# Kernel tuning notes

Measured on AMD Instinct MI355X. Metric: run time of the kernel, lower is better.

Reference implementation:

```python
import jax, jax.numpy as jnp
import numpy as np

N_HEAD = 16


def setup_inputs() -> dict:
    key = jax.random.key(0)
    ks = jax.random.split(key, 5)
    B, T, C = 2, 2048, 1024
    s = 1.0 / np.sqrt(C)
    inp = {
        "x": jax.random.normal(ks[0], (B, T, C), dtype=jnp.float32),
        "Wq": jax.random.normal(ks[1], (C, C), dtype=jnp.float32) * s,
        "bq": jnp.zeros((C,), dtype=jnp.float32),
        "Wk": jax.random.normal(ks[2], (C, C), dtype=jnp.float32) * s,
        "bk": jnp.zeros((C,), dtype=jnp.float32),
        "Wv": jax.random.normal(ks[3], (C, C), dtype=jnp.float32) * s,
        "bv": jnp.zeros((C,), dtype=jnp.float32),
        "Wp": jax.random.normal(ks[4], (C, C), dtype=jnp.float32) * s,
        "bp": jnp.zeros((C,), dtype=jnp.float32),
    }
    return inp


def reference(x, Wq, bq, Wk, bk, Wv, bv, Wp, bp):
    B, T, C = x.shape
    H = N_HEAD
    D = C // H
    # linear projections (torch Linear: x @ W.T + b)
    q = (x @ Wq.T + bq).reshape(B, T, H, D)
    k = (x @ Wk.T + bk).reshape(B, T, H, D)
    v = (x @ Wv.T + bv).reshape(B, T, H, D)
    # scaled dot-product attention (NO causal mask in original forward)
    att = jnp.einsum("bthd,bshd->bhts", q, k) * (1.0 / np.sqrt(D))
    att = jax.nn.softmax(att, axis=-1)
    y = jnp.einsum("bhts,bshd->bthd", att, v).reshape(B, T, C)
    # output projection (dropouts are identity at p=0 / eval)
    return y @ Wp.T + bp
```

## Files before the change

kernel.cpp:

```cpp
#include <hip/hip_runtime.h>
#include <hip/hip_bf16.h>

typedef __attribute__((ext_vector_type(4))) float f32x4;
typedef __attribute__((ext_vector_type(16))) float f32x16;
typedef __attribute__((ext_vector_type(8))) short bf16x8;
typedef __attribute__((ext_vector_type(2))) unsigned int u32x2;

#define T_SEQ 2048
#define C_DIM 1024
#define NH 16
#define DHD 64
#define ROWB 136

__device__ __forceinline__ unsigned cvtpk_bf16(float lo, float hi) {
    unsigned r;
    asm("v_cvt_pk_bf16_f32 %0, %1, %2" : "=v"(r) : "v"(lo), "v"(hi));
    return r;
}

__device__ __forceinline__ float exp2_hw(float x) {
    float r;
    asm("v_exp_f32 %0, %1" : "=v"(r) : "v"(x));
    return r;
}

__device__ __forceinline__ void async_copy16(void* lds, const void* g) {
    __builtin_amdgcn_global_load_lds(
        (const __attribute__((address_space(1))) unsigned int*)(uintptr_t)g,
        (__attribute__((address_space(3))) unsigned int*)(unsigned int)(uintptr_t)lds,
        16, 0, 0);
}

__device__ __forceinline__ bf16x8 ld_frag8(const char* p) {
    union { float2 f[2]; bf16x8 v; } u;
    u.f[0] = *(const float2*)(p);
    u.f[1] = *(const float2*)(p + 8);
    return u.v;
}

__global__ __launch_bounds__(256) void cvt_all(const float* __restrict__ x,
                                               const float* __restrict__ Wq, const float* __restrict__ Wk,
                                               const float* __restrict__ Wv, const float* __restrict__ Wp,
                                               __hip_bfloat16* __restrict__ xb,
                                               __hip_bfloat16* __restrict__ wf,
                                               __hip_bfloat16* __restrict__ wpb) {
    int i = blockIdx.x * blockDim.x + threadIdx.x;
    const float* src; __hip_bfloat16* dst; int off;
    if (i < 1048576) { src = x; dst = xb; off = i; }
    else {
        int j = i - 1048576; int wi = j >> 18; off = j & 262143;
        switch (wi) {
            case 0:  src = Wq; dst = wf;           break;
            case 1:  src = Wk; dst = wf + 1048576; break;
            case 2:  src = Wv; dst = wf + 2097152; break;
            default: src = Wp; dst = wpb;          break;
        }
    }
    float4 v = *(const float4*)(src + (size_t)off * 4);
    union { __hip_bfloat16 h[4]; u32x2 u; } p;
    p.h[0] = __float2bfloat16(v.x); p.h[1] = __float2bfloat16(v.y);
    p.h[2] = __float2bfloat16(v.z); p.h[3] = __float2bfloat16(v.w);
    *(u32x2*)(dst + (size_t)off * 4) = p.u;
}

__global__ __launch_bounds__(512) void gemm_qkv(const __hip_bfloat16* __restrict__ A,
                                                const __hip_bfloat16* __restrict__ Bw,
                                                const float* __restrict__ biasq,
                                                const float* __restrict__ biask,
                                                const float* __restrict__ biasv,
                                                __hip_bfloat16* __restrict__ oq,
                                                __hip_bfloat16* __restrict__ okk,
                                                __hip_bfloat16* __restrict__ ovt) {
    __shared__ __align__(16) char lds[131072];

    const int wg = ((int)blockIdx.x & 7) * 32 + ((int)blockIdx.x >> 3);
    const int m0 = (wg & 31) * 128;
    const int n0 = (wg >> 5) * 384;

    const int tid = threadIdx.x;
    const int w = tid >> 6, l = tid & 63;
    const int wr = w >> 2, wc = w & 3;
    const int lg = l >> 4, lr = l & 15;

    const int sr0 = tid >> 3;
    const int sc0 = (tid & 7) * 16;
    const int gc0 = sc0 ^ ((sr0 & 7) << 4);
    const size_t goff = (size_t)sr0 * 2048 + gc0;

    const char* Ag = (const char*)A + (size_t)m0 * 2048;
    const char* Bg = (const char*)Bw + (size_t)n0 * 2048;

    auto STAGE_A = [&](int buf, int half, int kt) {
        const char* g = Ag + (size_t)(half * 64) * 2048 + kt * 128 + goff;
        char* d = lds + (buf * 2 + half) * 8192 + w * 1024;
        async_copy16(d, g);
    };
    auto STAGE_B = [&](int buf, int half, int kt) {
        #pragma unroll
        for (int p = 0; p < 3; p++) {
            const char* g = Bg + (size_t)(half * 192 + p * 64) * 2048 + kt * 128 + goff;
            char* d = lds + 32768 + (buf * 2 + half) * 24576 + p * 8192 + w * 1024;
            async_copy16(d, g);
        }
    };

    const int sw = (lr & 7) << 4;
    auto LDA = [&](bf16x8* af, int buf) {
        const char* base = lds + (buf * 2 + wr) * 8192;
        #pragma unroll
        for (int m = 0; m < 4; m++) {
            const int r = m * 16 + lr;
            #pragma unroll
            for (int kk = 0; kk < 2; kk++)
                af[m * 2 + kk] = *(const bf16x8*)(base + r * 128 + ((kk * 64 + lg * 16) ^ sw));
        }
    };
    auto LDB = [&](bf16x8* bfv, int buf, int nq) {
        const char* base = lds + 32768 + (buf * 2 + (wc >> 1)) * 24576;
        #pragma unroll
        for (int n = 0; n < 2; n++) {
            const int r = (wc & 1) * 96 + (nq * 2 + n) * 16 + lr;
            #pragma unroll
            for (int kk = 0; kk < 2; kk++)
                bfv[n * 2 + kk] = *(const bf16x8*)(base + r * 128 + ((kk * 64 + lg * 16) ^ sw));
        }
    };

    f32x4 acc[4][6] = {};
    auto MF = [&](const bf16x8* af, const bf16x8* bfv, int nq) {
        #pragma unroll
        for (int m = 0; m < 4; m++)
            #pragma unroll
            for (int n = 0; n < 2; n++)
                #pragma unroll
                for (int kk = 0; kk < 2; kk++)
                    acc[m][nq * 2 + n] = __builtin_amdgcn_mfma_f32_16x16x32_bf16(
                        af[m * 2 + kk], bfv[n * 2 + kk], acc[m][nq * 2 + n], 0, 0, 0);
    };

#define PH_OPEN()  __builtin_amdgcn_sched_barrier(0); \
                   __builtin_amdgcn_s_barrier(); \
                   asm volatile("s_waitcnt lgkmcnt(0)" ::: "memory"); \
                   __builtin_amdgcn_sched_barrier(0); \
                   __builtin_amdgcn_s_setprio(1);
#define PH_CLOSE() __builtin_amdgcn_s_setprio(0); \
                   __builtin_amdgcn_sched_barrier(0); \
                   __builtin_amdgcn_s_barrier();
#define PH_CLOSE_VM2() __builtin_amdgcn_s_setprio(0); \
                   asm volatile("s_waitcnt vmcnt(2)" ::: "memory"); \
                   __builtin_amdgcn_sched_barrier(0); \
                   __builtin_amdgcn_s_barrier();
#define PH_CLOSE_VM5() __builtin_amdgcn_s_setprio(0); \
                   asm volatile("s_waitcnt vmcnt(5)" ::: "memory"); \
                   __builtin_amdgcn_sched_barrier(0); \
                   __builtin_amdgcn_s_barrier();

    bf16x8 af[8], bfA[4], bfB[4], bfC[4];

    STAGE_B(0, 0, 0); STAGE_B(0, 1, 0); STAGE_A(0, 0, 0); STAGE_A(0, 1, 0);
    STAGE_A(1, 0, 1); STAGE_A(1, 1, 1); STAGE_B(1, 0, 1);
    asm volatile("s_waitcnt vmcnt(5)" ::: "memory");
    __builtin_amdgcn_sched_barrier(0);
    __builtin_amdgcn_s_barrier();

    for (int it = 0; it < 8; ++it) {
        const int t1 = 2 * it + 1;
        const int c2 = (2 * it + 2 < 16) ? 2 * it + 2 : 14;
        const int c3 = (2 * it + 3 < 16) ? 2 * it + 3 : 15;
        const int b2 = c2 & 1, b3 = c3 & 1;

        LDA(af, 0); LDB(bfA, 0, 0);
        STAGE_B(1, 1, t1);
        PH_OPEN(); MF(af, bfA, 0); PH_CLOSE();
        LDB(bfB, 0, 1);
        STAGE_A(b2, 0, c2); STAGE_A(b2, 1, c2);
        PH_OPEN(); MF(af, bfB, 1); PH_CLOSE();
        LDB(bfC, 0, 2);
        PH_OPEN(); MF(af, bfC, 2); PH_CLOSE_VM2();

        LDA(af, 1); LDB(bfA, 1, 0);
        STAGE_B(b2, 0, c2);
        PH_OPEN(); MF(af, bfA, 0); PH_CLOSE();
        LDB(bfB, 1, 1);
        STAGE_B(b2, 1, c2); STAGE_A(b3, 0, c3); STAGE_A(b3, 1, c3);
        PH_OPEN(); MF(af, bfB, 1); PH_CLOSE();
        LDB(bfC, 1, 2);
        STAGE_B(b3, 0, c3);
        PH_OPEN(); MF(af, bfC, 2); PH_CLOSE_VM5();
    }
#undef PH_OPEN
#undef PH_CLOSE
#undef PH_CLOSE_VM2
#undef PH_CLOSE_VM5

    #pragma unroll
    for (int m = 0; m < 4; m++) {
        const int rowb = m0 + wr * 64 + m * 16 + lg * 4;
        const int b = rowb >> 11, t0r = rowb & 2047;
        #pragma unroll
        for (int nf = 0; nf < 6; nf++) {
            const int col = n0 + wc * 96 + nf * 16 + lr;
            const int proj = col >> 10;
            const int colL = col & 1023;
            const int hh = colL >> 6, dd = colL & 63;
            if (proj < 2) {
                const float* bias = (proj == 0) ? biasq : biask;
                const float bsc = (proj == 0) ? 0.125f * 1.4426950408889634f : 1.0f;
                __hip_bfloat16* dst = (proj == 0) ? oq : okk;
                #pragma unroll
                for (int rr = 0; rr < 4; rr++) {
                    const int row = rowb + rr;
                    float val = (acc[m][nf][rr] + bias[colL]) * bsc;
                    dst[(((size_t)(b * NH + hh)) * T_SEQ + (row & 2047)) * DHD + dd] = __float2bfloat16(val);
                }
            } else {
                const float bv = biasv[colL];
                union { __hip_bfloat16 h[4]; u32x2 u; } p;
                #pragma unroll
                for (int rr = 0; rr < 4; rr++)
                    p.h[rr] = __float2bfloat16(acc[m][nf][rr] + bv);
                *(u32x2*)&ovt[(((size_t)(b * NH + hh)) * DHD + dd) * T_SEQ + t0r] = p.u;
            }
        }
    }
}

__global__ __launch_bounds__(512) void gemm_proj2(const __hip_bfloat16* __restrict__ A,
                                                  const __hip_bfloat16* __restrict__ Bw,
                                                  const float* __restrict__ biasp,
                                                  float* __restrict__ outf) {
    __shared__ __align__(16) char lds[65536];

    const int wg = ((int)blockIdx.x & 7) * 32 + ((int)blockIdx.x >> 3);
    const int m0 = (wg & 31) * 128;
    const int n0 = (wg >> 5) * 128;

    const int tid = threadIdx.x;
    const int w = tid >> 6, l = tid & 63;
    const int wr = w >> 2, wc = w & 3;
    const int lg = l >> 4, lr = l & 15;

    const int sr0 = tid >> 3;
    const int sc0 = (tid & 7) * 16;
    const int gc0 = sc0 ^ ((sr0 & 7) << 4);
    const size_t goff = (size_t)sr0 * 2048 + gc0;

    const char* Ag = (const char*)A + (size_t)m0 * 2048;
    const char* Bg = (const char*)Bw + (size_t)n0 * 2048;

    auto STAGE_A = [&](int buf, int half, int kt) {
        const char* g = Ag + (size_t)(half * 64) * 2048 + kt * 128 + goff;
        char* d = lds + (buf * 2 + half) * 8192 + w * 1024;
        async_copy16(d, g);
    };
    auto STAGE_B = [&](int buf, int half, int kt) {
        const char* g = Bg + (size_t)(half * 64) * 2048 + kt * 128 + goff;
        char* d = lds + 32768 + (buf * 2 + half) * 8192 + w * 1024;
        async_copy16(d, g);
    };

    const int sw = (lr & 7) << 4;
    auto LDA = [&](bf16x8* af, int buf) {
        const char* base = lds + (buf * 2 + wr) * 8192;
        #pragma unroll
        for (int m = 0; m < 4; m++) {
            const int r = m * 16 + lr;
            #pragma unroll
            for (int kk = 0; kk < 2; kk++)
                af[m * 2 + kk] = *(const bf16x8*)(base + r * 128 + ((kk * 64 + lg * 16) ^ sw));
        }
    };
    auto LDB = [&](bf16x8* bfv, int buf, int n) {
        const char* base = lds + 32768 + (buf * 2 + (wc >> 1)) * 8192;
        const int r = (wc & 1) * 32 + n * 16 + lr;
        #pragma unroll
        for (int kk = 0; kk < 2; kk++)
            bfv[kk] = *(const bf16x8*)(base + r * 128 + ((kk * 64 + lg * 16) ^ sw));
    };

    f32x4 acc[4][2] = {};
    auto MF = [&](const bf16x8* af, const bf16x8* bfv, int n) {
        #pragma unroll
        for (int m = 0; m < 4; m++)
            #pragma unroll
            for (int kk = 0; kk < 2; kk++)
                acc[m][n] = __builtin_amdgcn_mfma_f32_16x16x32_bf16(
                    af[m * 2 + kk], bfv[kk], acc[m][n], 0, 0, 0);
    };

#define PH_OPEN()  __builtin_amdgcn_sched_barrier(0); \
                   __builtin_amdgcn_s_barrier(); \
                   asm volatile("s_waitcnt lgkmcnt(0)" ::: "memory"); \
                   __builtin_amdgcn_sched_barrier(0); \
                   __builtin_amdgcn_s_setprio(1);
#define PH_CLOSE() __builtin_amdgcn_s_setprio(0); \
                   __builtin_amdgcn_sched_barrier(0); \
                   __builtin_amdgcn_s_barrier();
#define PH_CLOSE_VM2() __builtin_amdgcn_s_setprio(0); \
                   asm volatile("s_waitcnt vmcnt(2)" ::: "memory"); \
                   __builtin_amdgcn_sched_barrier(0); \
                   __builtin_amdgcn_s_barrier();

    bf16x8 af[8], bf0[2], bf1[2];

    STAGE_B(0, 0, 0); STAGE_B(0, 1, 0); STAGE_A(0, 0, 0); STAGE_A(0, 1, 0);
    STAGE_A(1, 0, 1); STAGE_A(1, 1, 1);
    asm volatile("s_waitcnt vmcnt(2)" ::: "memory");
    __builtin_amdgcn_sched_barrier(0);
    __builtin_amdgcn_s_barrier();

    for (int it = 0; it < 8; ++it) {
        const int t1 = 2 * it + 1;
        const int c2 = (2 * it + 2 < 16) ? 2 * it + 2 : 14;
        const int c3 = (2 * it + 3 < 16) ? 2 * it + 3 : 15;
        const int b2 = c2 & 1, b3 = c3 & 1;

        LDA(af, 0); LDB(bf0, 0, 0);
        STAGE_B(1, 0, t1); STAGE_B(1, 1, t1);
        PH_OPEN(); MF(af, bf0, 0); PH_CLOSE();
        LDB(bf1, 0, 1);
        STAGE_A(b2, 0, c2); STAGE_A(b2, 1, c2);
        PH_OPEN(); MF(af, bf1, 1); PH_CLOSE_VM2();

        LDA(af, 1); LDB(bf0, 1, 0);
        STAGE_B(b2, 0, c2); STAGE_B(b2, 1, c2);
        PH_OPEN(); MF(af, bf0, 0); PH_CLOSE();
        LDB(bf1, 1, 1);
        STAGE_A(b3, 0, c3); STAGE_A(b3, 1, c3);
        PH_OPEN(); MF(af, bf1, 1); PH_CLOSE_VM2();
    }
#undef PH_OPEN
#undef PH_CLOSE
#undef PH_CLOSE_VM2

    #pragma unroll
    for (int m = 0; m < 4; m++)
        #pragma unroll
        for (int n = 0; n < 2; n++)
            #pragma unroll
            for (int r = 0; r < 4; r++) {
                int row = m0 + wr * 64 + m * 16 + lg * 4 + r;
                int col = n0 + wc * 32 + n * 16 + lr;
                outf[(size_t)row * C_DIM + col] = acc[m][n][r] + biasp[col];
            }
}

__global__ __launch_bounds__(256) void attn12(const __hip_bfloat16* __restrict__ Q,
                                              const __hip_bfloat16* __restrict__ K,
                                              const __hip_bfloat16* __restrict__ Vt,
                                              __hip_bfloat16* __restrict__ Y) {
    const int bid = blockIdx.x;
    const int xcd = bid & 7, slot = bid >> 3;
    const int head = xcd * 4 + (slot & 3);
    const int qblk = slot >> 2;

    const int tid = threadIdx.x;
    const int w = tid >> 6, l = tid & 63;
    const int lq = l & 31, hi = l >> 5;
    const int q0 = qblk * 128 + w * 32;

    __shared__ __align__(16) char ldsa[52736];
    float* bc = (float*)(ldsa + 52224);

    const char* Kb = (const char*)(K + (size_t)head * T_SEQ * DHD);
    const char* Vb = (const char*)(Vt + (size_t)head * DHD * T_SEQ);

    bf16x8 qf[4];
    {
        const char* qrow = (const char*)(Q + ((size_t)head * T_SEQ + q0 + lq) * DHD);
        #pragma unroll
        for (int t = 0; t < 4; t++) qf[t] = *(const bf16x8*)(qrow + t * 32 + hi * 16);
    }

    f32x16 yacc[2] = {};
    float ls0 = 0.f, ls1 = 0.f, ls2 = 0.f, ls3 = 0.f;

    const int o0 = (2 * w) * 1024 + l * 16;
    const int o1 = o0 + 1024;
    const int r0 = o0 >> 7, c0b = o0 & 127;
    const int r1 = o1 >> 7, c1b = o1 & 127;
    const int wadr0 = r0 * ROWB + c0b;
    const int wadr1 = r1 * ROWB + c1b;
    const char* vsrc0 = Vb + (size_t)r0 * (T_SEQ * 2) + c0b;
    const char* vsrc1 = Vb + (size_t)r1 * (T_SEQ * 2) + c1b;

    float4 kreg0, kreg1, vreg0, vreg1;
    auto stage_load = [&](int tile) {
        const char* kb2 = Kb + (size_t)tile * 8192;
        kreg0 = *(const float4*)(kb2 + o0);
        kreg1 = *(const float4*)(kb2 + o1);
        vreg0 = *(const float4*)(vsrc0 + (size_t)tile * 128);
        vreg1 = *(const float4*)(vsrc1 + (size_t)tile * 128);
    };
    auto stage_write = [&](int buf) {
        char* ks = ldsa + buf * 8704;
        char* vs = ldsa + 26112 + buf * 8704;
        *(float2*)(ks + wadr0)     = make_float2(kreg0.x, kreg0.y);
        *(float2*)(ks + wadr0 + 8) = make_float2(kreg0.z, kreg0.w);
        *(float2*)(ks + wadr1)     = make_float2(kreg1.x, kreg1.y);
        *(float2*)(ks + wadr1 + 8) = make_float2(kreg1.z, kreg1.w);
        *(float2*)(vs + wadr0)     = make_float2(vreg0.x, vreg0.y);
        *(float2*)(vs + wadr0 + 8) = make_float2(vreg0.z, vreg0.w);
        *(float2*)(vs + wadr1)     = make_float2(vreg1.x, vreg1.y);
        *(float2*)(vs + wadr1 + 8) = make_float2(vreg1.z, vreg1.w);
    };

    auto qk = [&](int buf, f32x16& s0h, f32x16& s1h) {
        s0h = f32x16{}; s1h = f32x16{};
        const char* base0 = ldsa + buf * 8704 + lq * ROWB + hi * 16;
        const char* base1 = base0 + 32 * ROWB;
        __builtin_amdgcn_s_setprio(1);
        #pragma unroll
        for (int t = 0; t < 4; t++) {
            bf16x8 kf0 = ld_frag8(base0 + t * 32);
            s0h = __builtin_amdgcn_mfma_f32_32x32x16_bf16(kf0, qf[t], s0h, 0, 0, 0);
        }
        #pragma unroll
        for (int t = 0; t < 4; t++) {
            bf16x8 kf1 = ld_frag8(base1 + t * 32);
            s1h = __builtin_amdgcn_mfma_f32_32x32x16_bf16(kf1, qf[t], s1h, 0, 0, 0);
        }
        __builtin_amdgcn_s_setprio(0);
    };

    auto sm_exp = [&](f32x16& a, f32x16& b) {
        #pragma unroll
        for (int r = 0; r < 16; r += 4) {
            a[r + 0] = exp2_hw(a[r + 0]); a[r + 1] = exp2_hw(a[r + 1]);
            a[r + 2] = exp2_hw(a[r + 2]); a[r + 3] = exp2_hw(a[r + 3]);
            b[r + 0] = exp2_hw(b[r + 0]); b[r + 1] = exp2_hw(b[r + 1]);
            b[r + 2] = exp2_hw(b[r + 2]); b[r + 3] = exp2_hw(b[r + 3]);
            ls0 += a[r + 0] + b[r + 0];
            ls1 += a[r + 1] + b[r + 1];
            ls2 += a[r + 2] + b[r + 2];
            ls3 += a[r + 3] + b[r + 3];
        }
    };

    auto pv = [&](int buf, const f32x16& a, const f32x16& b) {
        unsigned pw0[8], pw1[8];
        #pragma unroll
        for (int M = 0; M < 4; M++) {
            const int u = M * 4;
            pw0[M] = cvtpk_bf16(a[u + 0], a[u + 1]);
            pw1[M] = cvtpk_bf16(a[u + 2], a[u + 3]);
            pw0[M + 4] = cvtpk_bf16(b[u + 0], b[u + 1]);
            pw1[M + 4] = cvtpk_bf16(b[u + 2], b[u + 3]);
        }
        const char* vb0 = ldsa + 26112 + buf * 8704 + lq * ROWB + hi * 16;
        __builtin_amdgcn_s_setprio(1);
        #pragma unroll
        for (int t = 0; t < 4; t++) {
            u32x2 s0p = __builtin_amdgcn_permlane32_swap(pw0[2 * t], pw0[2 * t + 1], false, false);
            u32x2 s1p = __builtin_amdgcn_permlane32_swap(pw1[2 * t], pw1[2 * t + 1], false, false);
            union { unsigned u[4]; bf16x8 v; } af;
            af.u[0] = s0p.x; af.u[1] = s1p.x; af.u[2] = s0p.y; af.u[3] = s1p.y;
            #pragma unroll
            for (int dh = 0; dh < 2; dh++) {
                bf16x8 vf = ld_frag8(vb0 + dh * (32 * ROWB) + t * 32);
                yacc[dh] = __builtin_amdgcn_mfma_f32_32x32x16_bf16(af.v, vf, yacc[dh], 0, 0, 0);
            }
        }
        __builtin_amdgcn_s_setprio(0);
    };

    f32x16 sA0, sA1, sB0, sB1;
    stage_load(0); stage_write(0);
    stage_load(1); stage_write(1);
    stage_load(2);
    __syncthreads();
    qk(0, sA0, sA1);

    for (int t = 0; t < 32; t += 2) {
        qk((t + 1) % 3, sB0, sB1);
        if (t + 2 < 32) {
            asm volatile("s_waitcnt vmcnt(0)" ::: "memory");
            stage_write((t + 2) % 3);
            if (t + 3 < 32) stage_load(t + 3);
        }
        sm_exp(sA0, sA1);
        pv(t % 3, sA0, sA1);
        asm volatile("s_waitcnt lgkmcnt(0)" ::: "memory");
        __builtin_amdgcn_s_barrier();
        __builtin_amdgcn_sched_barrier(0);

        const int t1 = t + 1;
        if (t1 + 1 < 32) qk((t1 + 1) % 3, sA0, sA1);
        if (t1 + 2 < 32) {
            asm volatile("s_waitcnt vmcnt(0)" ::: "memory");
            stage_write((t1 + 2) % 3);
            if (t1 + 3 < 32) stage_load(t1 + 3);
        }
        sm_exp(sB0, sB1);
        pv(t1 % 3, sB0, sB1);
        asm volatile("s_waitcnt lgkmcnt(0)" ::: "memory");
        __builtin_amdgcn_s_barrier();
        __builtin_amdgcn_sched_barrier(0);
    }

    float lsum = (ls0 + ls1) + (ls2 + ls3);
    lsum += __shfl_xor(lsum, 32);
    float inv = 1.0f / lsum;
    if (hi == 0) bc[w * 32 + lq] = inv;
    asm volatile("s_waitcnt lgkmcnt(0)" ::: "memory");
    __builtin_amdgcn_sched_barrier(0);

    const int b = head >> 4, h16 = head & 15;
    const size_t rowbase = (size_t)b * T_SEQ + q0;
    #pragma unroll
    for (int r = 0; r < 16; r++) {
        const int crow = (r & 3) + 8 * (r >> 2) + 4 * hi;
        const float iv = bc[w * 32 + crow];
        const size_t row = rowbase + crow;
        Y[row * C_DIM + h16 * DHD + lq]      = __float2bfloat16(yacc[0][r] * iv);
        Y[row * C_DIM + h16 * DHD + 32 + lq] = __float2bfloat16(yacc[1][r] * iv);
    }
}

extern "C" void kernel_launch(void* const* d_in, const int* in_sizes, int n_in,
                              void* d_out, int out_size, void* d_ws, size_t ws_size,
                              hipStream_t stream) {
    (void)in_sizes; (void)n_in; (void)out_size; (void)ws_size;
    const float* x  = (const float*)d_in[0];
    const float* Wq = (const float*)d_in[1];
    const float* bq = (const float*)d_in[2];
    const float* Wk = (const float*)d_in[3];
    const float* bk = (const float*)d_in[4];
    const float* Wv = (const float*)d_in[5];
    const float* bv = (const float*)d_in[6];
    const float* Wp = (const float*)d_in[7];
    const float* bp = (const float*)d_in[8];
    float* out = (float*)d_out;

    char* ws = (char*)d_ws;
    const size_t MC = (size_t)4096 * C_DIM;
    const size_t CC = (size_t)C_DIM * C_DIM;
    __hip_bfloat16* xb  = (__hip_bfloat16*)ws;  ws += MC * 2;
    __hip_bfloat16* wf  = (__hip_bfloat16*)ws;  ws += 3 * CC * 2;
    __hip_bfloat16* wpb = (__hip_bfloat16*)ws;  ws += CC * 2;
    __hip_bfloat16* qb  = (__hip_bfloat16*)ws;  ws += MC * 2;
    __hip_bfloat16* kb  = (__hip_bfloat16*)ws;  ws += MC * 2;
    __hip_bfloat16* vtb = (__hip_bfloat16*)ws;  ws += MC * 2;
    __hip_bfloat16* yb  = (__hip_bfloat16*)ws;  ws += MC * 2;

    cvt_all<<<8192, 256, 0, stream>>>(x, Wq, Wk, Wv, Wp, xb, wf, wpb);

    gemm_qkv<<<256, 512, 0, stream>>>(xb, wf, bq, bk, bv, qb, kb, vtb);

    attn12<<<512, 256, 0, stream>>>(qb, kb, vtb, yb);

    gemm_proj2<<<256, 512, 0, stream>>>(yb, wpb, bp, out);
}
```

Measured before the change: 112.7 us.

## Load V fragments directly from global into double-buffered registers, bypassing LDS

The attention kernel no longer stages V tiles through shared memory. Each wave loads its V MFMA fragments straight from global memory into two register buffers, one per ping-pong tile, prefetched one step ahead. The waitcnt is relaxed so the eight V loads can stay in flight while K is written to LDS. This halves the LDS footprint and removes the V LDS writes and reads. In exchange every wave fetches the full V tile on its own, which multiplies global/L2 traffic for V by the number of waves. It also adds about 64 VGPRs per thread, which may lower occupancy.

```diff
diff --git a/kernel.cpp b/kernel.cpp
--- a/kernel.cpp
+++ b/kernel.cpp
@@ -345,7 +345,7 @@
             }
 }
 
-__global__ __launch_bounds__(256) void attn12(const __hip_bfloat16* __restrict__ Q,
+__global__ __launch_bounds__(256) void attn13(const __hip_bfloat16* __restrict__ Q,
                                               const __hip_bfloat16* __restrict__ K,
                                               const __hip_bfloat16* __restrict__ Vt,
                                               __hip_bfloat16* __restrict__ Y) {
@@ -359,8 +359,8 @@
     const int lq = l & 31, hi = l >> 5;
     const int q0 = qblk * 128 + w * 32;
 
-    __shared__ __align__(16) char ldsa[52736];
-    float* bc = (float*)(ldsa + 52224);
+    __shared__ __align__(16) char ldsa[26624];
+    float* bc = (float*)(ldsa + 26112);
 
     const char* Kb = (const char*)(K + (size_t)head * T_SEQ * DHD);
     const char* Vb = (const char*)(Vt + (size_t)head * DHD * T_SEQ);
@@ -381,28 +381,29 @@
     const int r1 = o1 >> 7, c1b = o1 & 127;
     const int wadr0 = r0 * ROWB + c0b;
     const int wadr1 = r1 * ROWB + c1b;
-    const char* vsrc0 = Vb + (size_t)r0 * (T_SEQ * 2) + c0b;
-    const char* vsrc1 = Vb + (size_t)r1 * (T_SEQ * 2) + c1b;
-
-    float4 kreg0, kreg1, vreg0, vreg1;
+
+    float4 kreg0, kreg1;
     auto stage_load = [&](int tile) {
         const char* kb2 = Kb + (size_t)tile * 8192;
         kreg0 = *(const float4*)(kb2 + o0);
         kreg1 = *(const float4*)(kb2 + o1);
-        vreg0 = *(const float4*)(vsrc0 + (size_t)tile * 128);
-        vreg1 = *(const float4*)(vsrc1 + (size_t)tile * 128);
     };
     auto stage_write = [&](int buf) {
         char* ks = ldsa + buf * 8704;
-        char* vs = ldsa + 26112 + buf * 8704;
         *(float2*)(ks + wadr0)     = make_float2(kreg0.x, kreg0.y);
         *(float2*)(ks + wadr0 + 8) = make_float2(kreg0.z, kreg0.w);
         *(float2*)(ks + wadr1)     = make_float2(kreg1.x, kreg1.y);
         *(float2*)(ks + wadr1 + 8) = make_float2(kreg1.z, kreg1.w);
-        *(float2*)(vs + wadr0)     = make_float2(vreg0.x, vreg0.y);
-        *(float2*)(vs + wadr0 + 8) = make_float2(vreg0.z, vreg0.w);
-        *(float2*)(vs + wadr1)     = make_float2(vreg1.x, vreg1.y);
-        *(float2*)(vs + wadr1 + 8) = make_float2(vreg1.z, vreg1.w);
+    };
+
+    const char* Vfb = Vb + (size_t)lq * (T_SEQ * 2) + hi * 16;
+    auto load_vf = [&](bf16x8* vf, int tile) {
+        const char* p = Vfb + (size_t)tile * 128;
+        #pragma unroll
+        for (int t = 0; t < 4; t++)
+            #pragma unroll
+            for (int dh = 0; dh < 2; dh++)
+                vf[t * 2 + dh] = *(const bf16x8*)(p + (size_t)dh * 32 * (T_SEQ * 2) + t * 32);
     };
 
     auto qk = [&](int buf, f32x16& s0h, f32x16& s1h) {
@@ -437,7 +438,7 @@
         }
     };
 
-    auto pv = [&](int buf, const f32x16& a, const f32x16& b) {
+    auto pv = [&](const bf16x8* vf, const f32x16& a, const f32x16& b) {
         unsigned pw0[8], pw1[8];
         #pragma unroll
         for (int M = 0; M < 4; M++) {
@@ -447,7 +448,6 @@
             pw0[M + 4] = cvtpk_bf16(b[u + 0], b[u + 1]);
             pw1[M + 4] = cvtpk_bf16(b[u + 2], b[u + 3]);
         }
-        const char* vb0 = ldsa + 26112 + buf * 8704 + lq * ROWB + hi * 16;
         __builtin_amdgcn_s_setprio(1);
         #pragma unroll
         for (int t = 0; t < 4; t++) {
@@ -456,30 +456,34 @@
             union { unsigned u[4]; bf16x8 v; } af;
             af.u[0] = s0p.x; af.u[1] = s1p.x; af.u[2] = s0p.y; af.u[3] = s1p.y;
             #pragma unroll
-            for (int dh = 0; dh < 2; dh++) {
-                bf16x8 vf = ld_frag8(vb0 + dh * (32 * ROWB) + t * 32);
-                yacc[dh] = __builtin_amdgcn_mfma_f32_32x32x16_bf16(af.v, vf, yacc[dh], 0, 0, 0);
-            }
+            for (int dh = 0; dh < 2; dh++)
+                yacc[dh] = __builtin_amdgcn_mfma_f32_32x32x16_bf16(af.v, vf[t * 2 + dh], yacc[dh], 0, 0, 0);
         }
         __builtin_amdgcn_s_setprio(0);
     };
 
     f32x16 sA0, sA1, sB0, sB1;
+    bf16x8 vfA[8], vfB[8];
     stage_load(0); stage_write(0);
     stage_load(1); stage_write(1);
     stage_load(2);
+    load_vf(vfA, 0);
+    load_vf(vfB, 1);
     __syncthreads();
     qk(0, sA0, sA1);
 
     for (int t = 0; t < 32; t += 2) {
         qk((t + 1) % 3, sB0, sB1);
         if (t + 2 < 32) {
-            asm volatile("s_waitcnt vmcnt(0)" ::: "memory");
+            asm volatile("s_waitcnt vmcnt(8)" ::: "memory");
             stage_write((t + 2) % 3);
             if (t + 3 < 32) stage_load(t + 3);
+        } else {
+            asm volatile("s_waitcnt vmcnt(0)" ::: "memory");
         }
         sm_exp(sA0, sA1);
-        pv(t % 3, sA0, sA1);
+        pv(vfA, sA0, sA1);
+        if (t + 2 < 32) load_vf(vfA, t + 2);
         asm volatile("s_waitcnt lgkmcnt(0)" ::: "memory");
         __builtin_amdgcn_s_barrier();
         __builtin_amdgcn_sched_barrier(0);
@@ -487,12 +491,15 @@
         const int t1 = t + 1;
         if (t1 + 1 < 32) qk((t1 + 1) % 3, sA0, sA1);
         if (t1 + 2 < 32) {
-            asm volatile("s_waitcnt vmcnt(0)" ::: "memory");
+            asm volatile("s_waitcnt vmcnt(8)" ::: "memory");
             stage_write((t1 + 2) % 3);
             if (t1 + 3 < 32) stage_load(t1 + 3);
+        } else {
+            asm volatile("s_waitcnt vmcnt(0)" ::: "memory");
         }
         sm_exp(sB0, sB1);
-        pv(t1 % 3, sB0, sB1);
+        pv(vfB, sB0, sB1);
+        if (t1 + 2 < 32) load_vf(vfB, t1 + 2);
         asm volatile("s_waitcnt lgkmcnt(0)" ::: "memory");
         __builtin_amdgcn_s_barrier();
         __builtin_amdgcn_sched_barrier(0);
@@ -547,7 +554,7 @@
 
     gemm_qkv<<<256, 512, 0, stream>>>(xb, wf, bq, bk, bv, qb, kb, vtb);
 
-    attn12<<<512, 256, 0, stream>>>(qb, kb, vtb, yb);
+    attn13<<<512, 256, 0, stream>>>(qb, kb, vtb, yb);
 
     gemm_proj2<<<256, 512, 0, stream>>>(yb, wpb, bp, out);
 }
```

Result: slower. 142.8 us (+26.8%).
